# Performance work log

Hardware: AMD Instinct MI355X
Metric: run time of the kernel (lower is better)

## Reference

```python
import jax, jax.numpy as jnp
import numpy as np

N = 10000      # nodes
E = 320000     # edges (before self loops)
IN = 256
HID = 64
H = 8
OUT = 64
NEG_SLOPE = 0.2


def setup_inputs() -> dict:
    key = jax.random.key(0)
    ks = jax.random.split(key, 12)
    def glorot(k, shape):
        fan = sum(shape) if len(shape) == 2 else int(np.prod(shape))
        return jax.random.normal(k, shape, jnp.float32) * np.sqrt(2.0 / fan)
    x = jax.random.normal(ks[0], (N, IN), jnp.float32)
    edge_index = jax.random.randint(ks[1], (2, E), 0, N, jnp.int32)
    # positive weights so log2 is finite
    edge_weight = jax.random.uniform(ks[2], (E,), jnp.float32, 0.1, 1.0)
    return {
        'x': x, 'edge_index': edge_index, 'edge_weight': edge_weight,
        'W1': glorot(ks[3], (IN, H * HID)),
        'as1': glorot(ks[4], (H, HID)), 'ad1': glorot(ks[5], (H, HID)),
        'b1': jnp.zeros((H * HID,), jnp.float32),
        'W2': glorot(ks[6], (H * HID, H * OUT)),
        'as2': glorot(ks[7], (H, OUT)), 'ad2': glorot(ks[8], (H, OUT)),
        'b2': jnp.zeros((H * OUT,), jnp.float32),
    }


def _gat_conv(x, src, dst, log2_ew, W, att_src, att_dst, bias, heads, ch):
    n = x.shape[0]
    h = (x @ W).reshape(n, heads, ch)                      # [N,H,C]
    al_src = jnp.einsum('nhc,hc->nh', h, att_src)          # [N,H]
    al_dst = jnp.einsum('nhc,hc->nh', h, att_dst)
    alpha = al_src[src] + al_dst[dst]                      # [E,H]
    alpha = jax.nn.leaky_relu(alpha, NEG_SLOPE)
    alpha = alpha + log2_ew[:, None]
    # segment softmax over destination nodes (self loops ensure nonempty segments)
    amax = jax.ops.segment_max(alpha, dst, num_segments=n)
    ex = jnp.exp(alpha - amax[dst])
    denom = jax.ops.segment_sum(ex, dst, num_segments=n)
    alpha = ex / denom[dst]                                # [E,H]
    msg = h[src] * alpha[:, :, None]                       # [E,H,C]
    out = jax.ops.segment_sum(msg, dst, num_segments=n)    # [N,H,C]
    return out.reshape(n, heads * ch) + bias


def reference(x, edge_index, edge_weight, W1, as1, ad1, b1, W2, as2, ad2, b2):
    n = x.shape[0]
    # add self loops with fill_value = 1.0 (log2(1) = 0)
    loops = jnp.arange(n, dtype=edge_index.dtype)
    src = jnp.concatenate([edge_index[0], loops])
    dst = jnp.concatenate([edge_index[1], loops])
    ew = jnp.concatenate([edge_weight, jnp.ones((n,), edge_weight.dtype)])
    log2_ew = jnp.log2(ew)
    h = _gat_conv(x, src, dst, log2_ew, W1, as1, ad1, b1, H, HID)
    h = jax.nn.relu(h)  # dropout skipped (eval mode)
    out = _gat_conv(h, src, dst, log2_ew, W2, as2, ad2, b2, H, OUT)
    return out
```

## Files before the change

kernel.cpp:

```cpp
#include <hip/hip_runtime.h>
#include <hip/hip_bf16.h>

#define NN 10000
#define EE 320000
#define ETOT (EE + NN)
#define CIN 256
#define HC 512
#define NHEAD 8
#define NEG 0.2f

using bf16x8 = __attribute__((ext_vector_type(8))) short;
using f32x4 = __attribute__((ext_vector_type(4))) float;
typedef unsigned short u16;
typedef unsigned int u32;

__device__ __forceinline__ u16 f2bf(float f) {
  __hip_bfloat16 b = __float2bfloat16(f);
  return *(u16*)&b;
}
__device__ __forceinline__ float bflo(u32 p) { return __uint_as_float(p << 16); }
__device__ __forceinline__ float bfhi(u32 p) { return __uint_as_float(p & 0xFFFF0000u); }

__global__ void detect_k(const u16* __restrict__ x, int* __restrict__ flag) {
  if (threadIdx.x == 0 && blockIdx.x == 0) {
    int isbf16 = 1;
    for (int i = 0; i < 512; i++) {
      unsigned e = (x[i] >> 7) & 0xFFu;
      if (e >= 0xC8u) { isbf16 = 0; break; }
    }
    *flag = isbf16;
  }
}

#define SX (NN * CIN)
#define SW1 (CIN * HC)
#define SW2 (HC * HC)
#define SATT (6 * 512)
__global__ void cvtall_k(const void* __restrict__ x, const void* __restrict__ w1,
                         const void* __restrict__ w2,
                         const void* a0, const void* a1, const void* a2,
                         const void* a3, const void* a4, const void* a5,
                         u16* __restrict__ xb, u16* __restrict__ w1b,
                         u16* __restrict__ w2b, float* __restrict__ attf,
                         const int* __restrict__ flag) {
  int i = blockIdx.x * blockDim.x + threadIdx.x;
  const bool bf = (*flag != 0);
  if (i < SX) {
    xb[i] = bf ? ((const u16*)x)[i] : f2bf(((const float*)x)[i]);
  } else if (i < SX + SW1) {
    int j = i - SX;
    w1b[j] = bf ? ((const u16*)w1)[j] : f2bf(((const float*)w1)[j]);
  } else if (i < SX + SW1 + SW2) {
    int j = i - SX - SW1;
    w2b[j] = bf ? ((const u16*)w2)[j] : f2bf(((const float*)w2)[j]);
  } else if (i < SX + SW1 + SW2 + SATT) {
    int j = i - SX - SW1 - SW2;
    const void* ps[6] = {a0, a1, a2, a3, a4, a5};
    const void* p = ps[j >> 9];
    int k = j & 511;
    attf[j] = bf ? __bfloat162float(((const __hip_bfloat16*)p)[k])
                 : ((const float*)p)[k];
  }
}

#define BM 128
#define BN 64
#define BK 32
#define APAD 40
#define BPAD 40

__global__ __launch_bounds__(256) void gemm_mfma(const u16* __restrict__ A,
                                                 const u16* __restrict__ B,
                                                 float* __restrict__ C,
                                                 int M, int K) {
  __shared__ u16 As[BM * APAD];
  __shared__ u16 Bs[BN * BPAD];
  const int bm = blockIdx.y * BM, bn = blockIdx.x * BN;
  const int t = threadIdx.x;
  const int wave = t >> 6, lane = t & 63;
  const int l15 = lane & 15, quad = lane >> 4;
  f32x4 acc[2][4] = {};
  for (int k0 = 0; k0 < K; k0 += BK) {
    {
      int row = t >> 1, half = t & 1;
      int gr = bm + row;
      int4 v0 = make_int4(0, 0, 0, 0), v1 = v0;
      if (gr < M) {
        const int4* gp = (const int4*)(A + (size_t)gr * K + k0 + half * 16);
        v0 = gp[0];
        v1 = gp[1];
      }
      int4* lp = (int4*)(As + row * APAD + half * 16);
      lp[0] = v0;
      lp[1] = v1;
    }
    {
      int n = t & 63;
#pragma unroll
      for (int j = 0; j < 4; j++) {
        int kp = (t >> 6) + j * 4;
        int k = kp * 2;
        u16 b0 = B[(size_t)(k0 + k) * HC + bn + n];
        u16 b1 = B[(size_t)(k0 + k + 1) * HC + bn + n];
        *(u32*)(Bs + n * BPAD + k) = (u32)b0 | ((u32)b1 << 16);
      }
    }
    __syncthreads();
    bf16x8 af[2], bfr[4];
#pragma unroll
    for (int rt = 0; rt < 2; rt++)
      af[rt] = *(const bf16x8*)(As + (wave * 32 + rt * 16 + l15) * APAD + quad * 8);
#pragma unroll
    for (int ct = 0; ct < 4; ct++)
      bfr[ct] = *(const bf16x8*)(Bs + (ct * 16 + l15) * BPAD + quad * 8);
#pragma unroll
    for (int rt = 0; rt < 2; rt++)
#pragma unroll
      for (int ct = 0; ct < 4; ct++)
        acc[rt][ct] = __builtin_amdgcn_mfma_f32_16x16x32_bf16(af[rt], bfr[ct],
                                                              acc[rt][ct], 0, 0, 0);
    __syncthreads();
  }
#pragma unroll
  for (int rt = 0; rt < 2; rt++) {
#pragma unroll
    for (int r = 0; r < 4; r++) {
      int row = bm + wave * 32 + rt * 16 + quad * 4 + r;
      if (row < M) {
#pragma unroll
        for (int ct = 0; ct < 4; ct++)
          C[(size_t)row * HC + bn + ct * 16 + l15] = acc[rt][ct][r];
      }
    }
  }
}

__global__ void logits_k(const float* __restrict__ hbuf,
                         const float* __restrict__ as_w,
                         const float* __restrict__ ad_w,
                         float* __restrict__ alsrc, float* __restrict__ aldst,
                         u16* __restrict__ hb) {
  int idx = blockIdx.x * blockDim.x + threadIdx.x;
  if (idx >= NN * NHEAD) return;
  int n = idx >> 3, h = idx & 7;
  const float4* hp = (const float4*)(hbuf + (size_t)n * HC + h * 64);
  const float4* aw = (const float4*)(as_w + h * 64);
  const float4* dw = (const float4*)(ad_w + h * 64);
  u32* hbp = (u32*)(hb + (size_t)n * HC + h * 64);
  float s = 0.f, d = 0.f;
#pragma unroll
  for (int c = 0; c < 16; c++) {
    float4 v = hp[c], a = aw[c], b = dw[c];
    s += v.x * a.x + v.y * a.y + v.z * a.z + v.w * a.w;
    d += v.x * b.x + v.y * b.y + v.z * b.z + v.w * b.w;
    hbp[c * 2] = (u32)f2bf(v.x) | ((u32)f2bf(v.y) << 16);
    hbp[c * 2 + 1] = (u32)f2bf(v.z) | ((u32)f2bf(v.w) << 16);
  }
  alsrc[idx] = s;
  aldst[idx] = d;
}

__global__ void count_k(const int* __restrict__ ei, int* __restrict__ counts) {
  int e = blockIdx.x * blockDim.x + threadIdx.x;
  if (e >= ETOT) return;
  int d = (e < EE) ? ei[EE + e] : (e - EE);
  atomicAdd(&counts[d], 1);
}

__global__ __launch_bounds__(1024) void scan_k(const int* __restrict__ counts,
                                               int* __restrict__ rowptr) {
  __shared__ int buf[1024];
  const int t = threadIdx.x;
  int loc[10];
  int s = 0;
#pragma unroll
  for (int j = 0; j < 10; j++) {
    int i = t * 10 + j;
    s += (i < NN) ? counts[i] : 0;
    loc[j] = s;
  }
  buf[t] = s;
  __syncthreads();
  for (int off = 1; off < 1024; off <<= 1) {
    int v = (t >= off) ? buf[t - off] : 0;
    __syncthreads();
    buf[t] += v;
    __syncthreads();
  }
  int base = (t > 0) ? buf[t - 1] : 0;
#pragma unroll
  for (int j = 0; j < 10; j++) {
    int i = t * 10 + j;
    if (i < NN) rowptr[i + 1] = base + loc[j];
  }
  if (t == 0) rowptr[0] = 0;
}

__global__ void fill_k(const int* __restrict__ ei, const void* __restrict__ ew,
                       const int* __restrict__ flag, const int* __restrict__ rowptr,
                       int* __restrict__ cursor, int* __restrict__ esrc,
                       float* __restrict__ elw) {
  int e = blockIdx.x * blockDim.x + threadIdx.x;
  if (e >= ETOT) return;
  int s, d;
  float lw;
  if (e < EE) {
    s = ei[e];
    d = ei[EE + e];
    float w = (*flag) ? __bfloat162float(((const __hip_bfloat16*)ew)[e])
                      : ((const float*)ew)[e];
    lw = log2f(w);
  } else {
    s = d = e - EE;
    lw = 0.f;
  }
  int pos = atomicAdd(&cursor[d], 1);
  int idx = rowptr[d] + pos;
  esrc[idx] = s;
  elw[idx] = lw;
}

template <bool RELU, bool FINAL>
__global__ __launch_bounds__(256) void agg_k(const u16* __restrict__ hb,
                                             const float* __restrict__ alsrc,
                                             const float* __restrict__ aldst,
                                             const int* __restrict__ rowptr,
                                             const int* __restrict__ esrc,
                                             const float* __restrict__ elw,
                                             const float* __restrict__ bias,
                                             u32* __restrict__ outB,
                                             float* __restrict__ outF,
                                             const int* __restrict__ flag) {
  const int n = blockIdx.x, t = threadIdx.x;
  __shared__ float red[256];
  __shared__ float sw[32 * NHEAD];
  __shared__ int ss[32];
  __shared__ float sm[NHEAD], sd[NHEAD], sal[NHEAD];
  if (t < NHEAD) sal[t] = aldst[n * NHEAD + t];
  __syncthreads();
  const int h = t & 7, eo = t >> 3;
  const int beg = rowptr[n], end = rowptr[n + 1];
  const float aln = sal[h];
  float m = -1e30f;
  for (int e = beg + eo; e < end; e += 32) {
    float a = alsrc[esrc[e] * NHEAD + h] + aln;
    a = (a > 0.f) ? a : NEG * a;
    a += elw[e];
    m = fmaxf(m, a);
  }
  red[t] = m;
  __syncthreads();
  for (int off = 128; off >= 8; off >>= 1) {
    if (t < off) red[t] = fmaxf(red[t], red[t + off]);
    __syncthreads();
  }
  if (t < NHEAD) sm[t] = red[t];
  __syncthreads();
  const float mh = sm[h];
  float sum = 0.f;
  for (int e = beg + eo; e < end; e += 32) {
    float a = alsrc[esrc[e] * NHEAD + h] + aln;
    a = (a > 0.f) ? a : NEG * a;
    a += elw[e];
    sum += expf(a - mh);
  }
  red[t] = sum;
  __syncthreads();
  for (int off = 128; off >= 8; off >>= 1) {
    if (t < off) red[t] += red[t + off];
    __syncthreads();
  }
  if (t < NHEAD) sd[t] = red[t];
  __syncthreads();
  const int hh = t >> 5;
  float acc0 = 0.f, acc1 = 0.f;
  for (int base = beg; base < end; base += 32) {
    int cnt = min(32, end - base);
    if (eo < cnt) {
      int e = base + eo;
      int s = esrc[e];
      float a = alsrc[s * NHEAD + h] + aln;
      a = (a > 0.f) ? a : NEG * a;
      a += elw[e];
      sw[eo * NHEAD + h] = expf(a - mh);
      if (h == 0) ss[eo] = s;
    }
    __syncthreads();
    for (int i = 0; i < cnt; i++) {
      int s = ss[i];
      u32 p = *(const u32*)(hb + (size_t)s * HC + 2 * t);
      float w = sw[i * NHEAD + hh];
      acc0 += w * bflo(p);
      acc1 += w * bfhi(p);
    }
    __syncthreads();
  }
  const float inv = 1.f / sd[hh];
  float v0 = acc0 * inv + bias[2 * t];
  float v1 = acc1 * inv + bias[2 * t + 1];
  if (RELU) {
    v0 = fmaxf(v0, 0.f);
    v1 = fmaxf(v1, 0.f);
  }
  if (FINAL && !(*flag)) {
    outF[(size_t)n * HC + 2 * t] = v0;
    outF[(size_t)n * HC + 2 * t + 1] = v1;
  } else {
    outB[(size_t)n * (HC / 2) + t] = (u32)f2bf(v0) | ((u32)f2bf(v1) << 16);
  }
}

static constexpr size_t algn(size_t x) { return (x + 255) & ~(size_t)255; }
static constexpr size_t oFlag = 0;
static constexpr size_t oXB = algn(oFlag + 256);
static constexpr size_t oW1B = algn(oXB + (size_t)SX * 2);
static constexpr size_t oW2B = algn(oW1B + (size_t)SW1 * 2);
static constexpr size_t oAtt = algn(oW2B + (size_t)SW2 * 2);
static constexpr size_t oH = algn(oAtt + (size_t)SATT * 4);
static constexpr size_t oHB = algn(oH + (size_t)NN * HC * 4);
static constexpr size_t oO1B = algn(oHB + (size_t)NN * HC * 2);
static constexpr size_t oAS = algn(oO1B + (size_t)NN * HC * 2);
static constexpr size_t oAD = algn(oAS + (size_t)NN * NHEAD * 4);
static constexpr size_t oRP = algn(oAD + (size_t)NN * NHEAD * 4);
static constexpr size_t oCur = algn(oRP + (size_t)(NN + 1) * 4);
static constexpr size_t oESrc = algn(oCur + (size_t)NN * 4);
static constexpr size_t oELW = algn(oESrc + (size_t)ETOT * 4);

extern "C" void kernel_launch(void* const* d_in, const int* in_sizes, int n_in,
                              void* d_out, int out_size, void* d_ws, size_t ws_size,
                              hipStream_t stream) {
  (void)in_sizes; (void)n_in; (void)out_size; (void)ws_size;
  const int* ei = (const int*)d_in[1];

  char* ws = (char*)d_ws;
  int* flag = (int*)(ws + oFlag);
  u16* xb = (u16*)(ws + oXB);
  u16* w1b = (u16*)(ws + oW1B);
  u16* w2b = (u16*)(ws + oW2B);
  float* attf = (float*)(ws + oAtt);
  float* as1f = attf, *ad1f = attf + 512, *b1f = attf + 1024;
  float* as2f = attf + 1536, *ad2f = attf + 2048, *b2f = attf + 2560;
  float* hbuf = (float*)(ws + oH);
  u16* hb = (u16*)(ws + oHB);
  u16* o1b = (u16*)(ws + oO1B);
  float* alsrc = (float*)(ws + oAS);
  float* aldst = (float*)(ws + oAD);
  int* rowptr = (int*)(ws + oRP);
  int* cursor = (int*)(ws + oCur);
  int* esrc = (int*)(ws + oESrc);
  float* elw = (float*)(ws + oELW);

  const int eb = (ETOT + 255) / 256;
  const int cvb = (SX + SW1 + SW2 + SATT + 255) / 256;

  detect_k<<<1, 64, 0, stream>>>((const u16*)d_in[0], flag);
  cvtall_k<<<cvb, 256, 0, stream>>>(d_in[0], d_in[3], d_in[7],
                                    d_in[4], d_in[5], d_in[6],
                                    d_in[8], d_in[9], d_in[10],
                                    xb, w1b, w2b, attf, flag);

  hipMemsetAsync(cursor, 0, (size_t)NN * 4, stream);
  count_k<<<eb, 256, 0, stream>>>(ei, cursor);
  scan_k<<<1, 1024, 0, stream>>>(cursor, rowptr);
  hipMemsetAsync(cursor, 0, (size_t)NN * 4, stream);
  fill_k<<<eb, 256, 0, stream>>>(ei, d_in[2], flag, rowptr, cursor, esrc, elw);

  gemm_mfma<<<dim3(HC / BN, (NN + BM - 1) / BM), 256, 0, stream>>>(xb, w1b, hbuf, NN, CIN);
  logits_k<<<(NN * NHEAD + 255) / 256, 256, 0, stream>>>(hbuf, as1f, ad1f, alsrc, aldst, hb);
  agg_k<true, false><<<NN, 256, 0, stream>>>(hb, alsrc, aldst, rowptr, esrc, elw,
                                             b1f, (u32*)o1b, nullptr, flag);

  gemm_mfma<<<dim3(HC / BN, (NN + BM - 1) / BM), 256, 0, stream>>>(o1b, w2b, hbuf, NN, HC);
  logits_k<<<(NN * NHEAD + 255) / 256, 256, 0, stream>>>(hbuf, as2f, ad2f, alsrc, aldst, hb);
  agg_k<false, true><<<NN, 256, 0, stream>>>(hb, alsrc, aldst, rowptr, esrc, elw,
                                             b2f, (u32*)d_out, (float*)d_out, flag);
}
```

Before: 318.1 us.

## Fuse logits into GEMM epilogue, pre-transpose weights, restructure aggregation and CSR build

Attention logits and the bf16 conversion of h now happen in the GEMM epilogue, with per-head shuffle reductions. This removes the fp32 h buffer and the separate logits kernel. Weights are transposed once to bf16 so the GEMM B tile loads as vectors. The CSR build merges edge counting into the conversion kernel and writes cursors from the scan, dropping the memsets. The aggregation kernel caches up to 256 edge logits in registers, reduces with wave shuffles, and gathers 8 channels per lane with wave-split edges reduced through shared memory; this costs extra LDS and registers.

Result: faster. 271.2 us (-14.7%).

```diff
diff --git a/kernel.cpp b/kernel.cpp
--- a/kernel.cpp
+++ b/kernel.cpp
@@ -9,6 +9,11 @@
 #define NHEAD 8
 #define NEG 0.2f
 
+#define SX (NN * CIN)
+#define SW1 (CIN * HC)
+#define SW2 (HC * HC)
+#define SATT (6 * 512)
+
 using bf16x8 = __attribute__((ext_vector_type(8))) short;
 using f32x4 = __attribute__((ext_vector_type(4))) float;
 typedef unsigned short u16;
@@ -21,46 +26,133 @@
 __device__ __forceinline__ float bflo(u32 p) { return __uint_as_float(p << 16); }
 __device__ __forceinline__ float bfhi(u32 p) { return __uint_as_float(p & 0xFFFF0000u); }
 
-__global__ void detect_k(const u16* __restrict__ x, int* __restrict__ flag) {
-  if (threadIdx.x == 0 && blockIdx.x == 0) {
-    int isbf16 = 1;
-    for (int i = 0; i < 512; i++) {
-      unsigned e = (x[i] >> 7) & 0xFFu;
-      if (e >= 0xC8u) { isbf16 = 0; break; }
-    }
-    *flag = isbf16;
-  }
-}
-
-#define SX (NN * CIN)
-#define SW1 (CIN * HC)
-#define SW2 (HC * HC)
-#define SATT (6 * 512)
-__global__ void cvtall_k(const void* __restrict__ x, const void* __restrict__ w1,
-                         const void* __restrict__ w2,
-                         const void* a0, const void* a1, const void* a2,
-                         const void* a3, const void* a4, const void* a5,
-                         u16* __restrict__ xb, u16* __restrict__ w1b,
-                         u16* __restrict__ w2b, float* __restrict__ attf,
-                         const int* __restrict__ flag) {
+__global__ void zdetect_k(const u16* __restrict__ x, int* __restrict__ flag,
+                          int* __restrict__ counts) {
+  int i = blockIdx.x * blockDim.x + threadIdx.x;
+  if (i < NN) counts[i] = 0;
+  if (blockIdx.x == 0 && threadIdx.x < 64) {
+    int bad = 0;
+    for (int j = threadIdx.x; j < 512; j += 64) {
+      unsigned e = (x[j] >> 7) & 0xFFu;
+      if (e >= 0xC8u) bad = 1;
+    }
+    unsigned long long b = __ballot(bad);
+    if (threadIdx.x == 0) *flag = (b == 0ull) ? 1 : 0;
+  }
+}
+
+__global__ void cvt_count_k(const void* __restrict__ x,
+                            const void* a0, const void* a1, const void* a2,
+                            const void* a3, const void* a4, const void* a5,
+                            const int* __restrict__ ei,
+                            u16* __restrict__ xb, float* __restrict__ attf,
+                            int* __restrict__ counts, const int* __restrict__ flag) {
   int i = blockIdx.x * blockDim.x + threadIdx.x;
   const bool bf = (*flag != 0);
   if (i < SX) {
     xb[i] = bf ? ((const u16*)x)[i] : f2bf(((const float*)x)[i]);
-  } else if (i < SX + SW1) {
+  } else if (i < SX + SATT) {
     int j = i - SX;
-    w1b[j] = bf ? ((const u16*)w1)[j] : f2bf(((const float*)w1)[j]);
-  } else if (i < SX + SW1 + SW2) {
-    int j = i - SX - SW1;
-    w2b[j] = bf ? ((const u16*)w2)[j] : f2bf(((const float*)w2)[j]);
-  } else if (i < SX + SW1 + SW2 + SATT) {
-    int j = i - SX - SW1 - SW2;
     const void* ps[6] = {a0, a1, a2, a3, a4, a5};
     const void* p = ps[j >> 9];
     int k = j & 511;
     attf[j] = bf ? __bfloat162float(((const __hip_bfloat16*)p)[k])
                  : ((const float*)p)[k];
   }
+  if (i < ETOT) {
+    int d = (i < EE) ? ei[EE + i] : (i - EE);
+    atomicAdd(&counts[d], 1);
+  }
+}
+
+__global__ __launch_bounds__(256) void wtrans_k(const void* __restrict__ w1,
+                                                const void* __restrict__ w2,
+                                                u16* __restrict__ w1t,
+                                                u16* __restrict__ w2t,
+                                                const int* __restrict__ flag) {
+  __shared__ u16 tile[64][72];
+  int b = blockIdx.x;
+  const void* src;
+  u16* dst;
+  int K, tk, tn;
+  if (b < 32) { src = w1; dst = w1t; K = CIN; tk = (b >> 3) * 64; tn = (b & 7) * 64; }
+  else { b -= 32; src = w2; dst = w2t; K = HC; tk = (b >> 3) * 64; tn = (b & 7) * 64; }
+  const bool bf = (*flag != 0);
+  const int t = threadIdx.x;
+  const int r = t >> 2, cb = (t & 3) * 16;
+  if (bf) {
+    const u16* s = (const u16*)src + (size_t)(tk + r) * HC + tn + cb;
+    *(int4*)&tile[r][cb] = ((const int4*)s)[0];
+    *(int4*)&tile[r][cb + 8] = ((const int4*)s)[1];
+  } else {
+    const float* s = (const float*)src + (size_t)(tk + r) * HC + tn + cb;
+#pragma unroll
+    for (int j = 0; j < 16; j++) tile[r][cb + j] = f2bf(s[j]);
+  }
+  __syncthreads();
+  union { u16 o[16]; int4 v[2]; } u;
+#pragma unroll
+  for (int j = 0; j < 16; j++) u.o[j] = tile[cb + j][r];
+  int4* dp = (int4*)(dst + (size_t)(tn + r) * K + tk + cb);
+  dp[0] = u.v[0];
+  dp[1] = u.v[1];
+}
+
+__global__ __launch_bounds__(1024) void scan_k(const int* __restrict__ counts,
+                                               int* __restrict__ rowptr,
+                                               int* __restrict__ wcur) {
+  __shared__ int buf[1024];
+  const int t = threadIdx.x;
+  int loc[10];
+  int s = 0;
+#pragma unroll
+  for (int j = 0; j < 10; j++) {
+    int i = t * 10 + j;
+    s += (i < NN) ? counts[i] : 0;
+    loc[j] = s;
+  }
+  buf[t] = s;
+  __syncthreads();
+  for (int off = 1; off < 1024; off <<= 1) {
+    int v = (t >= off) ? buf[t - off] : 0;
+    __syncthreads();
+    buf[t] += v;
+    __syncthreads();
+  }
+  int base = (t > 0) ? buf[t - 1] : 0;
+  int prev = 0;
+#pragma unroll
+  for (int j = 0; j < 10; j++) {
+    int i = t * 10 + j;
+    if (i < NN) {
+      rowptr[i + 1] = base + loc[j];
+      wcur[i] = base + prev;
+    }
+    prev = loc[j];
+  }
+  if (t == 0) rowptr[0] = 0;
+}
+
+__global__ void fill_k(const int* __restrict__ ei, const void* __restrict__ ew,
+                       const int* __restrict__ flag, int* __restrict__ wcur,
+                       int* __restrict__ esrc, float* __restrict__ elw) {
+  int e = blockIdx.x * blockDim.x + threadIdx.x;
+  if (e >= ETOT) return;
+  int s, d;
+  float lw;
+  if (e < EE) {
+    s = ei[e];
+    d = ei[EE + e];
+    float w = (*flag) ? __bfloat162float(((const __hip_bfloat16*)ew)[e])
+                      : ((const float*)ew)[e];
+    lw = log2f(w);
+  } else {
+    s = d = e - EE;
+    lw = 0.f;
+  }
+  int pos = atomicAdd(&wcur[d], 1);
+  esrc[pos] = s;
+  elw[pos] = lw;
 }
 
 #define BM 128
@@ -70,12 +162,17 @@
 #define BPAD 40
 
 __global__ __launch_bounds__(256) void gemm_mfma(const u16* __restrict__ A,
-                                                 const u16* __restrict__ B,
-                                                 float* __restrict__ C,
+                                                 const u16* __restrict__ Wt,
+                                                 const float* __restrict__ as_w,
+                                                 const float* __restrict__ ad_w,
+                                                 u16* __restrict__ hb,
+                                                 float* __restrict__ alsrc,
+                                                 float* __restrict__ aldst,
                                                  int M, int K) {
   __shared__ u16 As[BM * APAD];
   __shared__ u16 Bs[BN * BPAD];
-  const int bm = blockIdx.y * BM, bn = blockIdx.x * BN;
+  const int head = blockIdx.x;
+  const int bm = blockIdx.y * BM, bn = head * BN;
   const int t = threadIdx.x;
   const int wave = t >> 6, lane = t & 63;
   const int l15 = lane & 15, quad = lane >> 4;
@@ -95,15 +192,9 @@
       lp[1] = v1;
     }
     {
-      int n = t & 63;
-#pragma unroll
-      for (int j = 0; j < 4; j++) {
-        int kp = (t >> 6) + j * 4;
-        int k = kp * 2;
-        u16 b0 = B[(size_t)(k0 + k) * HC + bn + n];
-        u16 b1 = B[(size_t)(k0 + k + 1) * HC + bn + n];
-        *(u32*)(Bs + n * BPAD + k) = (u32)b0 | ((u32)b1 << 16);
-      }
+      int row = t >> 2, kq = (t & 3) * 8;
+      *(int4*)(Bs + row * BPAD + kq) =
+          *(const int4*)(Wt + (size_t)(bn + row) * K + k0 + kq);
     }
     __syncthreads();
     bf16x8 af[2], bfr[4];
@@ -121,103 +212,36 @@
                                                               acc[rt][ct], 0, 0, 0);
     __syncthreads();
   }
+  float asw[4], adw[4];
+#pragma unroll
+  for (int ct = 0; ct < 4; ct++) {
+    asw[ct] = as_w[head * 64 + ct * 16 + l15];
+    adw[ct] = ad_w[head * 64 + ct * 16 + l15];
+  }
 #pragma unroll
   for (int rt = 0; rt < 2; rt++) {
 #pragma unroll
     for (int r = 0; r < 4; r++) {
       int row = bm + wave * 32 + rt * 16 + quad * 4 + r;
-      if (row < M) {
-#pragma unroll
-        for (int ct = 0; ct < 4; ct++)
-          C[(size_t)row * HC + bn + ct * 16 + l15] = acc[rt][ct][r];
-      }
-    }
-  }
-}
-
-__global__ void logits_k(const float* __restrict__ hbuf,
-                         const float* __restrict__ as_w,
-                         const float* __restrict__ ad_w,
-                         float* __restrict__ alsrc, float* __restrict__ aldst,
-                         u16* __restrict__ hb) {
-  int idx = blockIdx.x * blockDim.x + threadIdx.x;
-  if (idx >= NN * NHEAD) return;
-  int n = idx >> 3, h = idx & 7;
-  const float4* hp = (const float4*)(hbuf + (size_t)n * HC + h * 64);
-  const float4* aw = (const float4*)(as_w + h * 64);
-  const float4* dw = (const float4*)(ad_w + h * 64);
-  u32* hbp = (u32*)(hb + (size_t)n * HC + h * 64);
-  float s = 0.f, d = 0.f;
-#pragma unroll
-  for (int c = 0; c < 16; c++) {
-    float4 v = hp[c], a = aw[c], b = dw[c];
-    s += v.x * a.x + v.y * a.y + v.z * a.z + v.w * a.w;
-    d += v.x * b.x + v.y * b.y + v.z * b.z + v.w * b.w;
-    hbp[c * 2] = (u32)f2bf(v.x) | ((u32)f2bf(v.y) << 16);
-    hbp[c * 2 + 1] = (u32)f2bf(v.z) | ((u32)f2bf(v.w) << 16);
-  }
-  alsrc[idx] = s;
-  aldst[idx] = d;
-}
-
-__global__ void count_k(const int* __restrict__ ei, int* __restrict__ counts) {
-  int e = blockIdx.x * blockDim.x + threadIdx.x;
-  if (e >= ETOT) return;
-  int d = (e < EE) ? ei[EE + e] : (e - EE);
-  atomicAdd(&counts[d], 1);
-}
-
-__global__ __launch_bounds__(1024) void scan_k(const int* __restrict__ counts,
-                                               int* __restrict__ rowptr) {
-  __shared__ int buf[1024];
-  const int t = threadIdx.x;
-  int loc[10];
-  int s = 0;
-#pragma unroll
-  for (int j = 0; j < 10; j++) {
-    int i = t * 10 + j;
-    s += (i < NN) ? counts[i] : 0;
-    loc[j] = s;
-  }
-  buf[t] = s;
-  __syncthreads();
-  for (int off = 1; off < 1024; off <<= 1) {
-    int v = (t >= off) ? buf[t - off] : 0;
-    __syncthreads();
-    buf[t] += v;
-    __syncthreads();
-  }
-  int base = (t > 0) ? buf[t - 1] : 0;
-#pragma unroll
-  for (int j = 0; j < 10; j++) {
-    int i = t * 10 + j;
-    if (i < NN) rowptr[i + 1] = base + loc[j];
-  }
-  if (t == 0) rowptr[0] = 0;
-}
-
-__global__ void fill_k(const int* __restrict__ ei, const void* __restrict__ ew,
-                       const int* __restrict__ flag, const int* __restrict__ rowptr,
-                       int* __restrict__ cursor, int* __restrict__ esrc,
-                       float* __restrict__ elw) {
-  int e = blockIdx.x * blockDim.x + threadIdx.x;
-  if (e >= ETOT) return;
-  int s, d;
-  float lw;
-  if (e < EE) {
-    s = ei[e];
-    d = ei[EE + e];
-    float w = (*flag) ? __bfloat162float(((const __hip_bfloat16*)ew)[e])
-                      : ((const float*)ew)[e];
-    lw = log2f(w);
-  } else {
-    s = d = e - EE;
-    lw = 0.f;
-  }
-  int pos = atomicAdd(&cursor[d], 1);
-  int idx = rowptr[d] + pos;
-  esrc[idx] = s;
-  elw[idx] = lw;
+      float ps = 0.f, pd = 0.f;
+#pragma unroll
+      for (int ct = 0; ct < 4; ct++) {
+        float v = acc[rt][ct][r];
+        ps += v * asw[ct];
+        pd += v * adw[ct];
+        if (row < M) hb[(size_t)row * HC + bn + ct * 16 + l15] = f2bf(v);
+      }
+#pragma unroll
+      for (int d = 1; d < 16; d <<= 1) {
+        ps += __shfl_xor(ps, d);
+        pd += __shfl_xor(pd, d);
+      }
+      if (l15 == 0 && row < M) {
+        alsrc[row * NHEAD + head] = ps;
+        aldst[row * NHEAD + head] = pd;
+      }
+    }
+  }
 }
 
 template <bool RELU, bool FINAL>
@@ -232,79 +256,145 @@
                                              float* __restrict__ outF,
                                              const int* __restrict__ flag) {
   const int n = blockIdx.x, t = threadIdx.x;
-  __shared__ float red[256];
+  const int lane = t & 63, wv = t >> 6;
+  const int h = t & 7, eo = t >> 3;
+  __shared__ float sred[32];
+  __shared__ float sd[NHEAD];
   __shared__ float sw[32 * NHEAD];
   __shared__ int ss[32];
-  __shared__ float sm[NHEAD], sd[NHEAD], sal[NHEAD];
-  if (t < NHEAD) sal[t] = aldst[n * NHEAD + t];
-  __syncthreads();
-  const int h = t & 7, eo = t >> 3;
-  const int beg = rowptr[n], end = rowptr[n + 1];
-  const float aln = sal[h];
+  __shared__ float red4[4][HC];
+  const int beg = rowptr[n];
+  const int deg = rowptr[n + 1] - beg;
+  const float aln = aldst[n * NHEAD + h];
+
+  float areg[8];
+  int sreg[8];
   float m = -1e30f;
-  for (int e = beg + eo; e < end; e += 32) {
+#pragma unroll
+  for (int c = 0; c < 8; c++) {
+    int j = c * 32 + eo;
+    float a = -1e30f;
+    int s = 0;
+    if (j < deg) {
+      int e = beg + j;
+      s = esrc[e];
+      a = alsrc[s * NHEAD + h] + aln;
+      a = (a > 0.f) ? a : NEG * a;
+      a += elw[e];
+      m = fmaxf(m, a);
+    }
+    areg[c] = a;
+    sreg[c] = s;
+  }
+  for (int j = 256 + eo; j < deg; j += 32) {
+    int e = beg + j;
     float a = alsrc[esrc[e] * NHEAD + h] + aln;
     a = (a > 0.f) ? a : NEG * a;
-    a += elw[e];
-    m = fmaxf(m, a);
-  }
-  red[t] = m;
-  __syncthreads();
-  for (int off = 128; off >= 8; off >>= 1) {
-    if (t < off) red[t] = fmaxf(red[t], red[t + off]);
-    __syncthreads();
-  }
-  if (t < NHEAD) sm[t] = red[t];
-  __syncthreads();
-  const float mh = sm[h];
+    m = fmaxf(m, a + elw[e]);
+  }
+  m = fmaxf(m, __shfl_xor(m, 8));
+  m = fmaxf(m, __shfl_xor(m, 16));
+  m = fmaxf(m, __shfl_xor(m, 32));
+  if (lane < 8) sred[wv * 8 + lane] = m;
+  __syncthreads();
+  const float mh = fmaxf(fmaxf(sred[h], sred[8 + h]), fmaxf(sred[16 + h], sred[24 + h]));
+  __syncthreads();
   float sum = 0.f;
-  for (int e = beg + eo; e < end; e += 32) {
+#pragma unroll
+  for (int c = 0; c < 8; c++) {
+    int j = c * 32 + eo;
+    if (j < deg) {
+      float w = expf(areg[c] - mh);
+      areg[c] = w;
+      sum += w;
+    }
+  }
+  for (int j = 256 + eo; j < deg; j += 32) {
+    int e = beg + j;
     float a = alsrc[esrc[e] * NHEAD + h] + aln;
     a = (a > 0.f) ? a : NEG * a;
-    a += elw[e];
-    sum += expf(a - mh);
-  }
-  red[t] = sum;
-  __syncthreads();
-  for (int off = 128; off >= 8; off >>= 1) {
-    if (t < off) red[t] += red[t + off];
-    __syncthreads();
-  }
-  if (t < NHEAD) sd[t] = red[t];
-  __syncthreads();
-  const int hh = t >> 5;
-  float acc0 = 0.f, acc1 = 0.f;
-  for (int base = beg; base < end; base += 32) {
-    int cnt = min(32, end - base);
-    if (eo < cnt) {
-      int e = base + eo;
+    sum += expf(a + elw[e] - mh);
+  }
+  sum += __shfl_xor(sum, 8);
+  sum += __shfl_xor(sum, 16);
+  sum += __shfl_xor(sum, 32);
+  if (lane < 8) sred[wv * 8 + lane] = sum;
+  __syncthreads();
+  if (t < 8) sd[t] = sred[t] + sred[8 + t] + sred[16 + t] + sred[24 + t];
+
+  const int hh = lane >> 3;
+  const int chbase = lane * 8;
+  float acc[8] = {};
+#pragma unroll
+  for (int c = 0; c < 8; c++) {
+    const int cb = c * 32;
+    if (cb < deg) {
+      if (cb + eo < deg) {
+        sw[eo * NHEAD + h] = areg[c];
+        if (h == 0) ss[eo] = sreg[c];
+      }
+      __syncthreads();
+      const int cnt = min(32, deg - cb);
+      for (int i = wv; i < cnt; i += 4) {
+        const int s = ss[i];
+        const float w = sw[i * NHEAD + hh];
+        const int4 p = *(const int4*)(hb + (size_t)s * HC + chbase);
+        const u32 p0 = (u32)p.x, p1 = (u32)p.y, p2 = (u32)p.z, p3 = (u32)p.w;
+        acc[0] += w * bflo(p0);
+        acc[1] += w * bfhi(p0);
+        acc[2] += w * bflo(p1);
+        acc[3] += w * bfhi(p1);
+        acc[4] += w * bflo(p2);
+        acc[5] += w * bfhi(p2);
+        acc[6] += w * bflo(p3);
+        acc[7] += w * bfhi(p3);
+      }
+      __syncthreads();
+    }
+  }
+  for (int cb = 256; cb < deg; cb += 32) {
+    if (cb + eo < deg) {
+      int e = beg + cb + eo;
       int s = esrc[e];
       float a = alsrc[s * NHEAD + h] + aln;
       a = (a > 0.f) ? a : NEG * a;
-      a += elw[e];
-      sw[eo * NHEAD + h] = expf(a - mh);
+      sw[eo * NHEAD + h] = expf(a + elw[e] - mh);
       if (h == 0) ss[eo] = s;
     }
     __syncthreads();
-    for (int i = 0; i < cnt; i++) {
-      int s = ss[i];
-      u32 p = *(const u32*)(hb + (size_t)s * HC + 2 * t);
-      float w = sw[i * NHEAD + hh];
-      acc0 += w * bflo(p);
-      acc1 += w * bfhi(p);
-    }
-    __syncthreads();
-  }
-  const float inv = 1.f / sd[hh];
-  float v0 = acc0 * inv + bias[2 * t];
-  float v1 = acc1 * inv + bias[2 * t + 1];
+    const int cnt = min(32, deg - cb);
+    for (int i = wv; i < cnt; i += 4) {
+      const int s = ss[i];
+      const float w = sw[i * NHEAD + hh];
+      const int4 p = *(const int4*)(hb + (size_t)s * HC + chbase);
+      const u32 p0 = (u32)p.x, p1 = (u32)p.y, p2 = (u32)p.z, p3 = (u32)p.w;
+      acc[0] += w * bflo(p0);
+      acc[1] += w * bfhi(p0);
+      acc[2] += w * bflo(p1);
+      acc[3] += w * bfhi(p1);
+      acc[4] += w * bflo(p2);
+      acc[5] += w * bfhi(p2);
+      acc[6] += w * bflo(p3);
+      acc[7] += w * bfhi(p3);
+    }
+    __syncthreads();
+  }
+#pragma unroll
+  for (int j = 0; j < 8; j++) red4[wv][chbase + j] = acc[j];
+  __syncthreads();
+  const int c0 = 2 * t, c1 = 2 * t + 1;
+  float v0 = red4[0][c0] + red4[1][c0] + red4[2][c0] + red4[3][c0];
+  float v1 = red4[0][c1] + red4[1][c1] + red4[2][c1] + red4[3][c1];
+  const float inv = 1.f / sd[t >> 5];
+  v0 = v0 * inv + bias[c0];
+  v1 = v1 * inv + bias[c1];
   if (RELU) {
     v0 = fmaxf(v0, 0.f);
     v1 = fmaxf(v1, 0.f);
   }
   if (FINAL && !(*flag)) {
-    outF[(size_t)n * HC + 2 * t] = v0;
-    outF[(size_t)n * HC + 2 * t + 1] = v1;
+    outF[(size_t)n * HC + c0] = v0;
+    outF[(size_t)n * HC + c1] = v1;
   } else {
     outB[(size_t)n * (HC / 2) + t] = (u32)f2bf(v0) | ((u32)f2bf(v1) << 16);
   }
@@ -313,17 +403,17 @@
 static constexpr size_t algn(size_t x) { return (x + 255) & ~(size_t)255; }
 static constexpr size_t oFlag = 0;
 static constexpr size_t oXB = algn(oFlag + 256);
-static constexpr size_t oW1B = algn(oXB + (size_t)SX * 2);
-static constexpr size_t oW2B = algn(oW1B + (size_t)SW1 * 2);
-static constexpr size_t oAtt = algn(oW2B + (size_t)SW2 * 2);
-static constexpr size_t oH = algn(oAtt + (size_t)SATT * 4);
-static constexpr size_t oHB = algn(oH + (size_t)NN * HC * 4);
+static constexpr size_t oW1T = algn(oXB + (size_t)SX * 2);
+static constexpr size_t oW2T = algn(oW1T + (size_t)SW1 * 2);
+static constexpr size_t oAtt = algn(oW2T + (size_t)SW2 * 2);
+static constexpr size_t oHB = algn(oAtt + (size_t)SATT * 4);
 static constexpr size_t oO1B = algn(oHB + (size_t)NN * HC * 2);
 static constexpr size_t oAS = algn(oO1B + (size_t)NN * HC * 2);
 static constexpr size_t oAD = algn(oAS + (size_t)NN * NHEAD * 4);
 static constexpr size_t oRP = algn(oAD + (size_t)NN * NHEAD * 4);
-static constexpr size_t oCur = algn(oRP + (size_t)(NN + 1) * 4);
-static constexpr size_t oESrc = algn(oCur + (size_t)NN * 4);
+static constexpr size_t oCnt = algn(oRP + (size_t)(NN + 1) * 4);
+static constexpr size_t oWcur = algn(oCnt + (size_t)NN * 4);
+static constexpr size_t oESrc = algn(oWcur + (size_t)NN * 4);
 static constexpr size_t oELW = algn(oESrc + (size_t)ETOT * 4);
 
 extern "C" void kernel_launch(void* const* d_in, const int* in_sizes, int n_in,
@@ -335,43 +425,39 @@
   char* ws = (char*)d_ws;
   int* flag = (int*)(ws + oFlag);
   u16* xb = (u16*)(ws + oXB);
-  u16* w1b = (u16*)(ws + oW1B);
-  u16* w2b = (u16*)(ws + oW2B);
+  u16* w1t = (u16*)(ws + oW1T);
+  u16* w2t = (u16*)(ws + oW2T);
   float* attf = (float*)(ws + oAtt);
   float* as1f = attf, *ad1f = attf + 512, *b1f = attf + 1024;
   float* as2f = attf + 1536, *ad2f = attf + 2048, *b2f = attf + 2560;
-  float* hbuf = (float*)(ws + oH);
   u16* hb = (u16*)(ws + oHB);
   u16* o1b = (u16*)(ws + oO1B);
   float* alsrc = (float*)(ws + oAS);
   float* aldst = (float*)(ws + oAD);
   int* rowptr = (int*)(ws + oRP);
-  int* cursor = (int*)(ws + oCur);
+  int* counts = (int*)(ws + oCnt);
+  int* wcur = (int*)(ws + oWcur);
   int* esrc = (int*)(ws + oESrc);
   float* elw = (float*)(ws + oELW);
 
   const int eb = (ETOT + 255) / 256;
-  const int cvb = (SX + SW1 + SW2 + SATT + 255) / 256;
-
-  detect_k<<<1, 64, 0, stream>>>((const u16*)d_in[0], flag);
-  cvtall_k<<<cvb, 256, 0, stream>>>(d_in[0], d_in[3], d_in[7],
-                                    d_in[4], d_in[5], d_in[6],
-                                    d_in[8], d_in[9], d_in[10],
-                                    xb, w1b, w2b, attf, flag);
-
-  hipMemsetAsync(cursor, 0, (size_t)NN * 4, stream);
-  count_k<<<eb, 256, 0, stream>>>(ei, cursor);
-  scan_k<<<1, 1024, 0, stream>>>(cursor, rowptr);
-  hipMemsetAsync(cursor, 0, (size_t)NN * 4, stream);
-  fill_k<<<eb, 256, 0, stream>>>(ei, d_in[2], flag, rowptr, cursor, esrc, elw);
-
-  gemm_mfma<<<dim3(HC / BN, (NN + BM - 1) / BM), 256, 0, stream>>>(xb, w1b, hbuf, NN, CIN);
-  logits_k<<<(NN * NHEAD + 255) / 256, 256, 0, stream>>>(hbuf, as1f, ad1f, alsrc, aldst, hb);
+  const int cvb = (SX + SATT + 255) / 256;
+
+  zdetect_k<<<(NN + 255) / 256, 256, 0, stream>>>((const u16*)d_in[0], flag, counts);
+  cvt_count_k<<<cvb, 256, 0, stream>>>(d_in[0], d_in[4], d_in[5], d_in[6],
+                                       d_in[8], d_in[9], d_in[10], ei,
+                                       xb, attf, counts, flag);
+  wtrans_k<<<96, 256, 0, stream>>>(d_in[3], d_in[7], w1t, w2t, flag);
+  scan_k<<<1, 1024, 0, stream>>>(counts, rowptr, wcur);
+  fill_k<<<eb, 256, 0, stream>>>(ei, d_in[2], flag, wcur, esrc, elw);
+
+  gemm_mfma<<<dim3(8, (NN + BM - 1) / BM), 256, 0, stream>>>(
+      xb, w1t, as1f, ad1f, hb, alsrc, aldst, NN, CIN);
   agg_k<true, false><<<NN, 256, 0, stream>>>(hb, alsrc, aldst, rowptr, esrc, elw,
                                              b1f, (u32*)o1b, nullptr, flag);
 
-  gemm_mfma<<<dim3(HC / BN, (NN + BM - 1) / BM), 256, 0, stream>>>(o1b, w2b, hbuf, NN, HC);
-  logits_k<<<(NN * NHEAD + 255) / 256, 256, 0, stream>>>(hbuf, as2f, ad2f, alsrc, aldst, hb);
+  gemm_mfma<<<dim3(8, (NN + BM - 1) / BM), 256, 0, stream>>>(
+      o1b, w2t, as2f, ad2f, hb, alsrc, aldst, NN, HC);
   agg_k<false, true><<<NN, 256, 0, stream>>>(hb, alsrc, aldst, rowptr, esrc, elw,
                                              b2f, (u32*)d_out, (float*)d_out, flag);
 }
```
